# Performance work log

Hardware: AMD Instinct MI355X
Metric: run time of the kernel (lower is better)

The kernel has to match this reference:

```python
import jax, jax.numpy as jnp
import numpy as np

EPS = 1e-15
SCALING = 2.0  # softmax scaling in AttentionReference.forward default


def _psd(xs, mask):
    """ESPnet get_power_spectral_density_matrix with fused einsum.
    xs:   (B, F, C, T) complex64
    mask: (B, F, C, T) float32
    returns psd: (B, F, C, C) complex64
    """
    m = mask.mean(axis=-2)                               # (B, F, T)
    m = m / (m.sum(axis=-1, keepdims=True) + EPS)        # normalize over T
    # fused masked covariance: sum_t m[t] * x[:,t] x[:,t]^H
    return jnp.einsum('bfct,bft,bfet->bfce', xs, m.astype(xs.dtype), jnp.conj(xs))


def _attention_reference(psd_in, mlp_w, mlp_b, gvec_w, gvec_b):
    """AttentionReference.forward. psd_in: (B,F,C,C) complex -> u: (B,C)."""
    C = psd_in.shape[-1]
    eye = jnp.eye(C, dtype=bool)
    psd = jnp.where(eye, jnp.zeros((), psd_in.dtype), psd_in)   # zero diagonal
    psd = jnp.swapaxes(psd.sum(axis=-1) / (C - 1), -1, -2)      # (B, C, F)
    psd_feat = jnp.sqrt(psd.real ** 2 + psd.imag ** 2)          # (B, C, F)
    mlp = jnp.tanh(psd_feat @ mlp_w + mlp_b)                    # (B, C, A)
    e = (mlp @ gvec_w + gvec_b)[..., 0]                         # (B, C)
    return jax.nn.softmax(SCALING * e, axis=-1)                 # (B, C)


def _mvdr_vector(psd_s, psd_n, u):
    """get_mvdr_vector: ws = inv(psd_n) @ psd_s / trace(.) then contract with u."""
    numerator = jnp.linalg.inv(psd_n) @ psd_s                   # (B, F, C, C)
    trace = jnp.einsum('bfcc->bf', numerator)
    ws_mat = numerator / (trace[..., None, None] + EPS)
    return jnp.einsum('bfec,bc->bfe', ws_mat, u.astype(ws_mat.dtype))  # (B, F, C)


def setup_inputs() -> dict:
    key = jax.random.key(0)
    ks = jax.random.split(key, 6)
    B, T, C, F, A = 8, 512, 8, 257, 320
    return {
        'data_real': jax.random.normal(ks[0], (B, T, C, F), jnp.float32),
        'data_imag': jax.random.normal(ks[1], (B, T, C, F), jnp.float32),
        'mask_speech': jax.random.uniform(ks[2], (B, F, C, T), jnp.float32),
        'mask_noise': jax.random.uniform(ks[3], (B, F, C, T), jnp.float32),
        'mlp_w': jax.random.normal(ks[4], (F, A), jnp.float32) / np.sqrt(F),
        'mlp_b': jnp.zeros((A,), jnp.float32),
        'gvec_w': jax.random.normal(ks[5], (A, 1), jnp.float32) / np.sqrt(A),
        'gvec_b': jnp.zeros((1,), jnp.float32),
        'ilens': jnp.full((B,), T, dtype=jnp.int32),
    }


def reference(data_real, data_imag, mask_speech, mask_noise,
              mlp_w, mlp_b, gvec_w, gvec_b, ilens):
    # data: (B,T,C,F) -> permute(0,3,2,1) -> (B,F,C,T)
    data = jnp.transpose(data_real + 1j * data_imag, (0, 3, 2, 1)).astype(jnp.complex64)
    psd_speech = _psd(data, mask_speech)    # (B,F,C,C)
    psd_noise = _psd(data, mask_noise)      # (B,F,C,C)
    u = _attention_reference(psd_speech, mlp_w, mlp_b, gvec_w, gvec_b)  # (B,C)
    ws = _mvdr_vector(psd_speech, psd_noise, u)                         # (B,F,C)
    # apply_beamforming_vector: conj(ws) . data over channels -> (B,F,T)
    enhanced = jnp.einsum('bfc,bfct->bft', jnp.conj(ws), data)
    enhanced = jnp.swapaxes(enhanced, -1, -2)                           # (B,T,F)
    # complex output packed as real (B,T,F,2)
    return jnp.stack([enhanced.real, enhanced.imag], axis=-1)
```

## Files before the change

### kernel.cpp

```cpp
#include <hip/hip_runtime.h>
#include <math.h>

#define TTOT 512
#define CCH 8
#define FFR 257
#define AAH 320
#define NBF 2056
#define BF2 2112
#define NTIL 16
#define TTILE 32
#define EPSF 1e-15f
#define WSB (FFR * 8)

#define OFF_MBS 0
#define OFF_MBN (OFF_MBS + NBF * 512)
#define OFF_PART (OFF_MBN + NBF * 512)
#define OFF_PSDS (OFF_PART + NTIL * 256 * BF2)
#define OFF_PSDN (OFF_PSDS + NBF * 128)
#define OFF_E (OFF_PSDN + NBF * 128)
#define OFF_WS (OFF_E + 64)

__global__ __launch_bounds__(128) void k_mask(
    const float* __restrict__ mask_s, const float* __restrict__ mask_n,
    float* __restrict__ mbar_s, float* __restrict__ mbar_n) {
  int bf = blockIdx.x;
  int tid = threadIdx.x;
  int lane = tid & 63, wv = tid >> 6;
  const float4* ms = (const float4*)(mask_s + (size_t)bf * CCH * TTOT);
  const float4* mn = (const float4*)(mask_n + (size_t)bf * CCH * TTOT);
  float4 ss = make_float4(0.f, 0.f, 0.f, 0.f);
  float4 sn = make_float4(0.f, 0.f, 0.f, 0.f);
#pragma unroll
  for (int c = 0; c < 8; ++c) {
    float4 a = ms[c * 128 + tid];
    ss.x += a.x; ss.y += a.y; ss.z += a.z; ss.w += a.w;
    float4 b = mn[c * 128 + tid];
    sn.x += b.x; sn.y += b.y; sn.z += b.z; sn.w += b.w;
  }
  float tots = (ss.x + ss.y) + (ss.z + ss.w);
  float totn = (sn.x + sn.y) + (sn.z + sn.w);
#pragma unroll
  for (int off = 32; off > 0; off >>= 1) {
    tots += __shfl_down(tots, off);
    totn += __shfl_down(totn, off);
  }
  __shared__ float reds[2], redn[2];
  if (lane == 0) { reds[wv] = tots; redn[wv] = totn; }
  __syncthreads();
  float invs = 0.125f / ((reds[0] + reds[1]) * 0.125f + EPSF);
  float invn = 0.125f / ((redn[0] + redn[1]) * 0.125f + EPSF);
  ((float4*)(mbar_s + (size_t)bf * TTOT))[tid] =
      make_float4(ss.x * invs, ss.y * invs, ss.z * invs, ss.w * invs);
  ((float4*)(mbar_n + (size_t)bf * TTOT))[tid] =
      make_float4(sn.x * invn, sn.y * invn, sn.z * invn, sn.w * invn);
}

__global__ __launch_bounds__(256, 3) void k_psd(
    const float* __restrict__ dr, const float* __restrict__ di,
    const float* __restrict__ mbar_s, const float* __restrict__ mbar_n,
    float* __restrict__ partial) {
  __shared__ float lms[64][33];
  __shared__ float lmn[64][33];
  int tid = threadIdx.x;
  int lane = tid & 63, wv = tid >> 6;
  int bfb = blockIdx.x, ttile = blockIdx.y;
  int t0 = ttile * TTILE;

  {
    int bfi = tid >> 2;
    int qo = (tid & 3) * 8;
    int bfg = bfb * 64 + bfi; if (bfg > NBF - 1) bfg = NBF - 1;
    const float* ps = mbar_s + (size_t)bfg * TTOT + t0 + qo;
    const float* pn = mbar_n + (size_t)bfg * TTOT + t0 + qo;
    float4 a = *(const float4*)ps;
    float4 b = *(const float4*)(ps + 4);
    float4 c = *(const float4*)pn;
    float4 d = *(const float4*)(pn + 4);
    lms[bfi][qo + 0] = a.x; lms[bfi][qo + 1] = a.y;
    lms[bfi][qo + 2] = a.z; lms[bfi][qo + 3] = a.w;
    lms[bfi][qo + 4] = b.x; lms[bfi][qo + 5] = b.y;
    lms[bfi][qo + 6] = b.z; lms[bfi][qo + 7] = b.w;
    lmn[bfi][qo + 0] = c.x; lmn[bfi][qo + 1] = c.y;
    lmn[bfi][qo + 2] = c.z; lmn[bfi][qo + 3] = c.w;
    lmn[bfi][qo + 4] = d.x; lmn[bfi][qo + 5] = d.y;
    lmn[bfi][qo + 6] = d.z; lmn[bfi][qo + 7] = d.w;
  }

  int bf = bfb * 64 + lane; if (bf > NBF - 1) bf = NBF - 1;
  int b = bf / FFR, f = bf - b * FFR;
  const float* br = dr + (size_t)b * TTOT * CCH * FFR + (size_t)t0 * CCH * FFR + f;
  const float* bi = di + (size_t)b * TTOT * CCH * FFR + (size_t)t0 * CCH * FFR + f;
  int qi = (wv >> 1) * 4, qj = (wv & 1) * 4;
  int ro[8];
#pragma unroll
  for (int k = 0; k < 4; ++k) { ro[k] = (qi + k) * FFR; ro[4 + k] = (qj + k) * FFR; }

  float acc[64];
#pragma unroll
  for (int g = 0; g < 64; ++g) acc[g] = 0.f;

  float A[16], B[16];

  auto LOADX = [&](float (&buf)[16], int tt) {
    const float* pr = br + (size_t)tt * (CCH * FFR);
    const float* pi_ = bi + (size_t)tt * (CCH * FFR);
#pragma unroll
    for (int k = 0; k < 8; ++k) {
      buf[k] = pr[ro[k]];
      buf[8 + k] = pi_[ro[k]];
    }
  };
  auto FMAX = [&](float (&buf)[16], int tt) {
    float m_s = lms[lane][tt];
    float m_n = lmn[lane][tt];
#pragma unroll
    for (int i4 = 0; i4 < 4; ++i4)
#pragma unroll
      for (int j4 = 0; j4 < 4; ++j4) {
        int p = i4 * 4 + j4;
        float pre = buf[i4] * buf[4 + j4] + buf[8 + i4] * buf[12 + j4];
        float pim = buf[8 + i4] * buf[4 + j4] - buf[i4] * buf[12 + j4];
        acc[p * 4 + 0] += m_s * pre;
        acc[p * 4 + 1] += m_s * pim;
        acc[p * 4 + 2] += m_n * pre;
        acc[p * 4 + 3] += m_n * pim;
      }
  };

  LOADX(A, 0);
  LOADX(B, 1);
  __syncthreads();
#pragma unroll
  for (int tt = 0; tt < TTILE; tt += 2) {
    FMAX(A, tt);
    if (tt + 2 < TTILE) LOADX(A, tt + 2);
    FMAX(B, tt + 1);
    if (tt + 3 < TTILE) LOADX(B, tt + 3);
  }

  size_t pbase = ((size_t)ttile * 256 + wv * 64) * BF2 + bfb * 64 + lane;
#pragma unroll
  for (int g = 0; g < 64; ++g)
    partial[pbase + (size_t)g * BF2] = acc[g];
}

__global__ __launch_bounds__(256) void k_reduce(
    const float* __restrict__ partial, float* __restrict__ psd_s,
    float* __restrict__ psd_n) {
  int lane = threadIdx.x & 63, wv = threadIdx.x >> 6;
  int bfb = blockIdx.x;
  int g = blockIdx.y * 4 + wv;
  int bf = bfb * 64 + lane;
  const float* src = partial + (size_t)g * BF2 + bfb * 64 + lane;
  float s = 0.f;
#pragma unroll
  for (int nt = 0; nt < NTIL; ++nt) s += src[(size_t)nt * 256 * BF2];
  if (bf < NBF) {
    int w = g >> 6, rem = g & 63, p = rem >> 2, comp = rem & 3;
    int i = (w >> 1) * 4 + (p >> 2);
    int j = (w & 1) * 4 + (p & 3);
    float* dst = (comp < 2) ? psd_s : psd_n;
    dst[(size_t)bf * 128 + (i * 8 + j) * 2 + (comp & 1)] = s;
  }
}

__global__ __launch_bounds__(320) void k2_attn(
    const float* __restrict__ psd_s, const float* __restrict__ mlp_w,
    const float* __restrict__ mlp_b, const float* __restrict__ gvec_w,
    float* __restrict__ e_out) {
  __shared__ float feat[FFR];
  __shared__ float wred[5];
  int bx = blockIdx.x;
  int b = bx >> 3, c = bx & 7;
  int tid = threadIdx.x;
  int lane = tid & 63, wv = tid >> 6;
  if (tid < FFR) {
    const float* p = psd_s + (((size_t)(b * FFR + tid)) * 8 + c) * 16;
    float sre = 0.f, sim = 0.f;
#pragma unroll
    for (int e = 0; e < 8; ++e) {
      if (e != c) { sre += p[e * 2]; sim += p[e * 2 + 1]; }
    }
    sre *= (1.0f / 7.0f);
    sim *= (1.0f / 7.0f);
    feat[tid] = sqrtf(sre * sre + sim * sim);
  }
  __syncthreads();
  float acc = mlp_b[tid];
#pragma unroll 8
  for (int f = 0; f < FFR; ++f) acc += feat[f] * mlp_w[f * AAH + tid];
  float v = tanhf(acc) * gvec_w[tid];
#pragma unroll
  for (int off = 32; off > 0; off >>= 1) v += __shfl_down(v, off);
  if (lane == 0) wred[wv] = v;
  __syncthreads();
  if (tid == 0) e_out[bx] = wred[0] + wred[1] + wred[2] + wred[3] + wred[4];
}

__global__ __launch_bounds__(256) void k3_mvdr(
    const float* __restrict__ psd_s, const float* __restrict__ psd_n,
    const float* __restrict__ e_in, const float* __restrict__ gvec_b,
    float* __restrict__ ws) {
  int lane = threadIdx.x & 63, wv = threadIdx.x >> 6;
  int bf = blockIdx.x * 4 + wv;
  int b = bf / FFR;
  int r = lane >> 3, c = lane & 7;
  float2 n = ((const float2*)(psd_n + (size_t)bf * 128))[lane];
  float2 s = ((const float2*)(psd_s + (size_t)bf * 128))[lane];

#pragma unroll
  for (int k = 0; k < 8; ++k) {
    float pvre = __shfl(n.x, k * 9), pvim = __shfl(n.y, k * 9);
    float dinv = 1.f / (pvre * pvre + pvim * pvim);
    float pire = pvre * dinv, piim = -pvim * dinv;
    if (r == k) {
      float2 nn = n, ss = s;
      n.x = nn.x * pire - nn.y * piim; n.y = nn.x * piim + nn.y * pire;
      s.x = ss.x * pire - ss.y * piim; s.y = ss.x * piim + ss.y * pire;
    }
    float fre = __shfl(n.x, r * 8 + k), fim = __shfl(n.y, r * 8 + k);
    float pnre = __shfl(n.x, k * 8 + c), pnim = __shfl(n.y, k * 8 + c);
    float psre = __shfl(s.x, k * 8 + c), psim = __shfl(s.y, k * 8 + c);
    if (r != k) {
      n.x -= fre * pnre - fim * pnim; n.y -= fre * pnim + fim * pnre;
      s.x -= fre * psre - fim * psim; s.y -= fre * psim + fim * psre;
    }
  }
  float trx = (r == c) ? s.x : 0.f, tryy = (r == c) ? s.y : 0.f;
#pragma unroll
  for (int off = 1; off < 64; off <<= 1) {
    trx += __shfl_xor(trx, off);
    tryy += __shfl_xor(tryy, off);
  }
  float val = 2.f * (e_in[b * 8 + c] + gvec_b[0]);
  float mx = val;
#pragma unroll
  for (int off = 1; off < 8; off <<= 1) mx = fmaxf(mx, __shfl_xor(mx, off));
  float pe = expf(val - mx);
  float psum = pe;
#pragma unroll
  for (int off = 1; off < 8; off <<= 1) psum += __shfl_xor(psum, off);
  float uc = pe / psum;
  float wre = s.x * uc, wim = s.y * uc;
#pragma unroll
  for (int off = 1; off < 8; off <<= 1) {
    wre += __shfl_xor(wre, off);
    wim += __shfl_xor(wim, off);
  }
  float tre = trx + EPSF, tim = tryy;
  float d2 = 1.f / (tre * tre + tim * tim);
  float owre = (wre * tre + wim * tim) * d2;
  float owim = (wim * tre - wre * tim) * d2;
  if (c == 0) ((float2*)ws)[(size_t)bf * 8 + r] = make_float2(owre, owim);
}

__global__ __launch_bounds__(256) void k4_beam(
    const float* __restrict__ dr, const float* __restrict__ di,
    const float* __restrict__ ws, float* __restrict__ out) {
  __shared__ float2 wsp[FFR * 9];
  int b = blockIdx.y;
  int t0 = blockIdx.x * 4;
  int tid = threadIdx.x;
  const float2* wsg = (const float2*)ws + (size_t)b * WSB;
  for (int i = tid; i < FFR * 8; i += 256) {
    int f = i >> 3, c = i & 7;
    wsp[f * 9 + c] = wsg[i];
  }
  __syncthreads();
  for (int ts = 0; ts < 4; ++ts) {
    int t = t0 + ts;
    const float* drb = dr + (size_t)(b * TTOT + t) * (CCH * FFR);
    const float* dib = di + (size_t)(b * TTOT + t) * (CCH * FFR);
    for (int f = tid; f < FFR; f += 256) {
      float are = 0.f, aim = 0.f;
#pragma unroll
      for (int c = 0; c < 8; ++c) {
        float xre = drb[c * FFR + f];
        float xim = dib[c * FFR + f];
        float2 w = wsp[f * 9 + c];
        are += w.x * xre + w.y * xim;
        aim += w.x * xim - w.y * xre;
      }
      ((float2*)out)[(size_t)(b * TTOT + t) * FFR + f] = make_float2(are, aim);
    }
  }
}

extern "C" void kernel_launch(void* const* d_in, const int* in_sizes, int n_in,
                              void* d_out, int out_size, void* d_ws, size_t ws_size,
                              hipStream_t stream) {
  const float* dr = (const float*)d_in[0];
  const float* di = (const float*)d_in[1];
  const float* mask_s = (const float*)d_in[2];
  const float* mask_n = (const float*)d_in[3];
  const float* mlp_w = (const float*)d_in[4];
  const float* mlp_b = (const float*)d_in[5];
  const float* gvec_w = (const float*)d_in[6];
  const float* gvec_b = (const float*)d_in[7];
  float* out = (float*)d_out;

  float* wsf = (float*)d_ws;
  float* mbar_s = wsf + OFF_MBS;
  float* mbar_n = wsf + OFF_MBN;
  float* part = wsf + OFF_PART;
  float* psd_s = wsf + OFF_PSDS;
  float* psd_n = wsf + OFF_PSDN;
  float* e_arr = wsf + OFF_E;
  float* wsv = wsf + OFF_WS;

  hipLaunchKernelGGL(k_mask, dim3(NBF), dim3(128), 0, stream,
                     mask_s, mask_n, mbar_s, mbar_n);
  hipLaunchKernelGGL(k_psd, dim3(33, NTIL), dim3(256), 0, stream,
                     dr, di, mbar_s, mbar_n, part);
  hipLaunchKernelGGL(k_reduce, dim3(33, 64), dim3(256), 0, stream,
                     part, psd_s, psd_n);
  hipLaunchKernelGGL(k2_attn, dim3(64), dim3(320), 0, stream,
                     psd_s, mlp_w, mlp_b, gvec_w, e_arr);
  hipLaunchKernelGGL(k3_mvdr, dim3(514), dim3(256), 0, stream,
                     psd_s, psd_n, e_arr, gvec_b, wsv);
  hipLaunchKernelGGL(k4_beam, dim3(128, 8), dim3(256), 0, stream, dr, di, wsv, out);
}
```

Baseline: 253.8 us.

## Exploit Hermitian symmetry in PSD accumulation and split attention MLP across blocks

The PSD kernel now computes only the upper-triangular 4x4 diagonal blocks (10 pairs each) plus the off-diagonal 4x4 block, so it accumulates 144 values per bin instead of 256. The reduce kernel fills in the lower triangle by conjugate mirroring. This cuts the FMA work and the size of the partial buffer. The time tile is halved to 16 to give more blocks, and the attention kernel is spread over 5 blocks per (b,c) whose results are combined with atomicAdd after a memset. In exchange, the waves are unbalanced (40 vs 64 accumulators per wave), there is an extra memset launch, and the atomic summation order is nondeterministic.

```diff
diff --git a/kernel.cpp b/kernel.cpp
--- a/kernel.cpp
+++ b/kernel.cpp
@@ -7,18 +7,22 @@
 #define AAH 320
 #define NBF 2056
 #define BF2 2112
-#define NTIL 16
-#define TTILE 32
+#define NTIL 32
+#define TTILE 16
+#define NG 144
 #define EPSF 1e-15f
 #define WSB (FFR * 8)
 
 #define OFF_MBS 0
 #define OFF_MBN (OFF_MBS + NBF * 512)
 #define OFF_PART (OFF_MBN + NBF * 512)
-#define OFF_PSDS (OFF_PART + NTIL * 256 * BF2)
+#define OFF_PSDS (OFF_PART + NTIL * NG * BF2)
 #define OFF_PSDN (OFF_PSDS + NBF * 128)
 #define OFF_E (OFF_PSDN + NBF * 128)
 #define OFF_WS (OFF_E + 64)
+
+__device__ __constant__ int d_pi[10] = {0,0,0,0,1,1,1,2,2,3};
+__device__ __constant__ int d_pj[10] = {0,1,2,3,1,2,3,2,3,3};
 
 __global__ __launch_bounds__(128) void k_mask(
     const float* __restrict__ mask_s, const float* __restrict__ mask_n,
@@ -55,93 +59,118 @@
       make_float4(sn.x * invn, sn.y * invn, sn.z * invn, sn.w * invn);
 }
 
-__global__ __launch_bounds__(256, 3) void k_psd(
+__global__ __launch_bounds__(192) void k_psd(
     const float* __restrict__ dr, const float* __restrict__ di,
     const float* __restrict__ mbar_s, const float* __restrict__ mbar_n,
     float* __restrict__ partial) {
-  __shared__ float lms[64][33];
-  __shared__ float lmn[64][33];
+  __shared__ float lms[64][TTILE + 1];
+  __shared__ float lmn[64][TTILE + 1];
   int tid = threadIdx.x;
-  int lane = tid & 63, wv = tid >> 6;
+  int lane = tid & 63, wq = tid >> 6;
   int bfb = blockIdx.x, ttile = blockIdx.y;
   int t0 = ttile * TTILE;
 
-  {
-    int bfi = tid >> 2;
-    int qo = (tid & 3) * 8;
+  for (int i = tid; i < 512; i += 192) {
+    int msel = i >> 8, rem = i & 255;
+    int bfi = rem >> 2, qo = (rem & 3) * 4;
     int bfg = bfb * 64 + bfi; if (bfg > NBF - 1) bfg = NBF - 1;
-    const float* ps = mbar_s + (size_t)bfg * TTOT + t0 + qo;
-    const float* pn = mbar_n + (size_t)bfg * TTOT + t0 + qo;
-    float4 a = *(const float4*)ps;
-    float4 b = *(const float4*)(ps + 4);
-    float4 c = *(const float4*)pn;
-    float4 d = *(const float4*)(pn + 4);
-    lms[bfi][qo + 0] = a.x; lms[bfi][qo + 1] = a.y;
-    lms[bfi][qo + 2] = a.z; lms[bfi][qo + 3] = a.w;
-    lms[bfi][qo + 4] = b.x; lms[bfi][qo + 5] = b.y;
-    lms[bfi][qo + 6] = b.z; lms[bfi][qo + 7] = b.w;
-    lmn[bfi][qo + 0] = c.x; lmn[bfi][qo + 1] = c.y;
-    lmn[bfi][qo + 2] = c.z; lmn[bfi][qo + 3] = c.w;
-    lmn[bfi][qo + 4] = d.x; lmn[bfi][qo + 5] = d.y;
-    lmn[bfi][qo + 6] = d.z; lmn[bfi][qo + 7] = d.w;
+    const float* src = (msel ? mbar_n : mbar_s) + (size_t)bfg * TTOT + t0 + qo;
+    float4 v = *(const float4*)src;
+    float (*l)[TTILE + 1] = msel ? lmn : lms;
+    l[bfi][qo + 0] = v.x; l[bfi][qo + 1] = v.y;
+    l[bfi][qo + 2] = v.z; l[bfi][qo + 3] = v.w;
   }
 
   int bf = bfb * 64 + lane; if (bf > NBF - 1) bf = NBF - 1;
   int b = bf / FFR, f = bf - b * FFR;
   const float* br = dr + (size_t)b * TTOT * CCH * FFR + (size_t)t0 * CCH * FFR + f;
   const float* bi = di + (size_t)b * TTOT * CCH * FFR + (size_t)t0 * CCH * FFR + f;
-  int qi = (wv >> 1) * 4, qj = (wv & 1) * 4;
-  int ro[8];
-#pragma unroll
-  for (int k = 0; k < 4; ++k) { ro[k] = (qi + k) * FFR; ro[4 + k] = (qj + k) * FFR; }
-
-  float acc[64];
-#pragma unroll
-  for (int g = 0; g < 64; ++g) acc[g] = 0.f;
-
-  float A[16], B[16];
-
-  auto LOADX = [&](float (&buf)[16], int tt) {
-    const float* pr = br + (size_t)tt * (CCH * FFR);
-    const float* pi_ = bi + (size_t)tt * (CCH * FFR);
-#pragma unroll
-    for (int k = 0; k < 8; ++k) {
-      buf[k] = pr[ro[k]];
-      buf[8 + k] = pi_[ro[k]];
-    }
-  };
-  auto FMAX = [&](float (&buf)[16], int tt) {
-    float m_s = lms[lane][tt];
-    float m_n = lmn[lane][tt];
-#pragma unroll
-    for (int i4 = 0; i4 < 4; ++i4)
-#pragma unroll
-      for (int j4 = 0; j4 < 4; ++j4) {
-        int p = i4 * 4 + j4;
-        float pre = buf[i4] * buf[4 + j4] + buf[8 + i4] * buf[12 + j4];
-        float pim = buf[8 + i4] * buf[4 + j4] - buf[i4] * buf[12 + j4];
+  __syncthreads();
+
+  size_t pbase = ((size_t)ttile * NG) * BF2 + bfb * 64 + lane;
+
+  if (wq < 2) {
+    int r0 = wq * 4;
+    float acc[40];
+#pragma unroll
+    for (int g = 0; g < 40; ++g) acc[g] = 0.f;
+    float A[8], B[8];
+    auto LOADX = [&](float (&buf)[8], int tt) {
+      const float* pr = br + (size_t)tt * (CCH * FFR);
+      const float* pi_ = bi + (size_t)tt * (CCH * FFR);
+#pragma unroll
+      for (int k = 0; k < 4; ++k) {
+        buf[k] = pr[(r0 + k) * FFR];
+        buf[4 + k] = pi_[(r0 + k) * FFR];
+      }
+    };
+    auto FMAX = [&](float (&buf)[8], int tt) {
+      float m_s = lms[lane][tt];
+      float m_n = lmn[lane][tt];
+#pragma unroll
+      for (int p = 0; p < 10; ++p) {
+        int i = d_pi[p], j = d_pj[p];
+        float pre = buf[i] * buf[j] + buf[4 + i] * buf[4 + j];
+        float pim = buf[4 + i] * buf[j] - buf[i] * buf[4 + j];
         acc[p * 4 + 0] += m_s * pre;
         acc[p * 4 + 1] += m_s * pim;
         acc[p * 4 + 2] += m_n * pre;
         acc[p * 4 + 3] += m_n * pim;
       }
-  };
-
-  LOADX(A, 0);
-  LOADX(B, 1);
-  __syncthreads();
-#pragma unroll
-  for (int tt = 0; tt < TTILE; tt += 2) {
-    FMAX(A, tt);
-    if (tt + 2 < TTILE) LOADX(A, tt + 2);
-    FMAX(B, tt + 1);
-    if (tt + 3 < TTILE) LOADX(B, tt + 3);
-  }
-
-  size_t pbase = ((size_t)ttile * 256 + wv * 64) * BF2 + bfb * 64 + lane;
-#pragma unroll
-  for (int g = 0; g < 64; ++g)
-    partial[pbase + (size_t)g * BF2] = acc[g];
+    };
+    LOADX(A, 0); LOADX(B, 1);
+#pragma unroll
+    for (int tt = 0; tt < TTILE; tt += 2) {
+      FMAX(A, tt);
+      if (tt + 2 < TTILE) LOADX(A, tt + 2);
+      FMAX(B, tt + 1);
+      if (tt + 3 < TTILE) LOADX(B, tt + 3);
+    }
+    size_t base = pbase + (size_t)(wq * 40) * BF2;
+#pragma unroll
+    for (int g = 0; g < 40; ++g) partial[base + (size_t)g * BF2] = acc[g];
+  } else {
+    float acc[64];
+#pragma unroll
+    for (int g = 0; g < 64; ++g) acc[g] = 0.f;
+    float A[16], B[16];
+    auto LOADX = [&](float (&buf)[16], int tt) {
+      const float* pr = br + (size_t)tt * (CCH * FFR);
+      const float* pi_ = bi + (size_t)tt * (CCH * FFR);
+#pragma unroll
+      for (int k = 0; k < 8; ++k) {
+        buf[k] = pr[k * FFR];
+        buf[8 + k] = pi_[k * FFR];
+      }
+    };
+    auto FMAX = [&](float (&buf)[16], int tt) {
+      float m_s = lms[lane][tt];
+      float m_n = lmn[lane][tt];
+#pragma unroll
+      for (int i = 0; i < 4; ++i)
+#pragma unroll
+        for (int jj = 0; jj < 4; ++jj) {
+          int p = i * 4 + jj;
+          float pre = buf[i] * buf[4 + jj] + buf[8 + i] * buf[12 + jj];
+          float pim = buf[8 + i] * buf[4 + jj] - buf[i] * buf[12 + jj];
+          acc[p * 4 + 0] += m_s * pre;
+          acc[p * 4 + 1] += m_s * pim;
+          acc[p * 4 + 2] += m_n * pre;
+          acc[p * 4 + 3] += m_n * pim;
+        }
+    };
+    LOADX(A, 0); LOADX(B, 1);
+#pragma unroll
+    for (int tt = 0; tt < TTILE; tt += 2) {
+      FMAX(A, tt);
+      if (tt + 2 < TTILE) LOADX(A, tt + 2);
+      FMAX(B, tt + 1);
+      if (tt + 3 < TTILE) LOADX(B, tt + 3);
+    }
+    size_t base = pbase + (size_t)80 * BF2;
+#pragma unroll
+    for (int g = 0; g < 64; ++g) partial[base + (size_t)g * BF2] = acc[g];
+  }
 }
 
 __global__ __launch_bounds__(256) void k_reduce(
@@ -154,47 +183,53 @@
   const float* src = partial + (size_t)g * BF2 + bfb * 64 + lane;
   float s = 0.f;
 #pragma unroll
-  for (int nt = 0; nt < NTIL; ++nt) s += src[(size_t)nt * 256 * BF2];
+  for (int nt = 0; nt < NTIL; ++nt) s += src[(size_t)nt * NG * BF2];
   if (bf < NBF) {
-    int w = g >> 6, rem = g & 63, p = rem >> 2, comp = rem & 3;
-    int i = (w >> 1) * 4 + (p >> 2);
-    int j = (w & 1) * 4 + (p & 3);
+    int i, j, comp;
+    if (g < 80) {
+      int q = g / 40, l = g - q * 40, p = l >> 2;
+      comp = l & 3;
+      i = d_pi[p] + q * 4; j = d_pj[p] + q * 4;
+    } else {
+      int l = g - 80, p = l >> 2;
+      comp = l & 3;
+      i = p >> 2; j = 4 + (p & 3);
+    }
     float* dst = (comp < 2) ? psd_s : psd_n;
-    dst[(size_t)bf * 128 + (i * 8 + j) * 2 + (comp & 1)] = s;
-  }
-}
-
-__global__ __launch_bounds__(320) void k2_attn(
+    int ci = comp & 1;
+    size_t base = (size_t)bf * 128;
+    dst[base + (i * 8 + j) * 2 + ci] = s;
+    dst[base + (j * 8 + i) * 2 + ci] = ci ? -s : s;
+  }
+}
+
+__global__ __launch_bounds__(64) void k2_attn(
     const float* __restrict__ psd_s, const float* __restrict__ mlp_w,
     const float* __restrict__ mlp_b, const float* __restrict__ gvec_w,
     float* __restrict__ e_out) {
   __shared__ float feat[FFR];
-  __shared__ float wred[5];
-  int bx = blockIdx.x;
-  int b = bx >> 3, c = bx & 7;
+  int bc = blockIdx.x;
+  int ach = blockIdx.y;
+  int b = bc >> 3, c = bc & 7;
   int tid = threadIdx.x;
-  int lane = tid & 63, wv = tid >> 6;
-  if (tid < FFR) {
-    const float* p = psd_s + (((size_t)(b * FFR + tid)) * 8 + c) * 16;
+  for (int f = tid; f < FFR; f += 64) {
+    const float* p = psd_s + (((size_t)(b * FFR + f)) * 8 + c) * 16;
     float sre = 0.f, sim = 0.f;
 #pragma unroll
     for (int e = 0; e < 8; ++e) {
       if (e != c) { sre += p[e * 2]; sim += p[e * 2 + 1]; }
     }
-    sre *= (1.0f / 7.0f);
-    sim *= (1.0f / 7.0f);
-    feat[tid] = sqrtf(sre * sre + sim * sim);
+    feat[f] = sqrtf(sre * sre + sim * sim) * (1.0f / 7.0f);
   }
   __syncthreads();
-  float acc = mlp_b[tid];
+  int a = ach * 64 + tid;
+  float acc = mlp_b[a];
 #pragma unroll 8
-  for (int f = 0; f < FFR; ++f) acc += feat[f] * mlp_w[f * AAH + tid];
-  float v = tanhf(acc) * gvec_w[tid];
+  for (int f = 0; f < FFR; ++f) acc += feat[f] * mlp_w[f * AAH + a];
+  float v = tanhf(acc) * gvec_w[a];
 #pragma unroll
   for (int off = 32; off > 0; off >>= 1) v += __shfl_down(v, off);
-  if (lane == 0) wred[wv] = v;
-  __syncthreads();
-  if (tid == 0) e_out[bx] = wred[0] + wred[1] + wred[2] + wred[3] + wred[4];
+  if (tid == 0) atomicAdd(&e_out[bc], v);
 }
 
 __global__ __launch_bounds__(256) void k3_mvdr(
@@ -310,11 +345,12 @@
 
   hipLaunchKernelGGL(k_mask, dim3(NBF), dim3(128), 0, stream,
                      mask_s, mask_n, mbar_s, mbar_n);
-  hipLaunchKernelGGL(k_psd, dim3(33, NTIL), dim3(256), 0, stream,
+  hipLaunchKernelGGL(k_psd, dim3(33, NTIL), dim3(192), 0, stream,
                      dr, di, mbar_s, mbar_n, part);
-  hipLaunchKernelGGL(k_reduce, dim3(33, 64), dim3(256), 0, stream,
+  hipLaunchKernelGGL(k_reduce, dim3(33, 36), dim3(256), 0, stream,
                      part, psd_s, psd_n);
-  hipLaunchKernelGGL(k2_attn, dim3(64), dim3(320), 0, stream,
+  hipMemsetAsync((void*)e_arr, 0, 64 * sizeof(float), stream);
+  hipLaunchKernelGGL(k2_attn, dim3(64, 5), dim3(64), 0, stream,
                      psd_s, mlp_w, mlp_b, gvec_w, e_arr);
   hipLaunchKernelGGL(k3_mvdr, dim3(514), dim3(256), 0, stream,
                      psd_s, psd_n, e_arr, gvec_b, wsv);
```

Result: slower. 511.1 us (+101.4%).
